# Kernel optimization log

Measured on AMD Instinct MI355X. Metric: run time of the kernel, lower is better.

## Reference

```python
import jax, jax.numpy as jnp
import numpy as np
from math import exp

C1 = 0.01 ** 2
C2 = 0.03 ** 2
WINDOW_SIZE = 11
SIGMA = 1.5

def make_window(window_size, channel, sigma=SIGMA):
    g = np.array([exp(-(x - window_size // 2) ** 2 / float(2 * sigma ** 2))
                  for x in range(window_size)], dtype=np.float32)
    g = g / g.sum()
    w2d = np.outer(g, g).astype(np.float32)  # [ws, ws]
    # depthwise kernel, OIHW with I=1 per group: [C, 1, ws, ws]
    return jnp.asarray(np.broadcast_to(w2d, (channel, 1, window_size, window_size)).copy())

def depthwise_conv(x, window, pad):
    C = x.shape[1]
    return jax.lax.conv_general_dilated(
        x, window, window_strides=(1, 1),
        padding=[(pad, pad), (pad, pad)],
        feature_group_count=C,
        dimension_numbers=('NCHW', 'OIHW', 'NCHW'))

def setup_inputs() -> dict:
    key = jax.random.key(0)
    k1, k2 = jax.random.split(key)
    B, C, H, W = 16, 3, 512, 512
    img1 = jax.random.uniform(k1, (B, C, H, W), dtype=jnp.float32)
    img2 = jax.random.uniform(k2, (B, C, H, W), dtype=jnp.float32)
    window = make_window(WINDOW_SIZE, C)
    return {"img1": img1, "img2": img2, "window": window}

def reference(img1, img2, window):
    pad = WINDOW_SIZE // 2
    mu1 = depthwise_conv(img1, window, pad)
    mu2 = depthwise_conv(img2, window, pad)
    mu1_sq = mu1 * mu1
    mu2_sq = mu2 * mu2
    mu1_mu2 = mu1 * mu2
    sigma1_sq = depthwise_conv(img1 * img1, window, pad) - mu1_sq
    sigma2_sq = depthwise_conv(img2 * img2, window, pad) - mu2_sq
    sigma12 = depthwise_conv(img1 * img2, window, pad) - mu1_mu2
    ssim_cs = (2 * sigma12 + C2) / (sigma1_sq + sigma2_sq + C2)
    ssim_l = (2 * mu1_mu2 + C1) / (mu1_sq + mu2_sq + C1)
    ssim_map = ssim_l * ssim_cs
    return jnp.mean(ssim_map)
```

## Files before the change

### kernel.cpp

```cpp
#include <hip/hip_runtime.h>


#define IMG_H 512
#define IMG_W 512
#define N_IMG 48
#define WS 11
#define PAD 5
#define CHUNK 16
#define NCHUNK (IMG_H / CHUNK)
#define NBLK (N_IMG * NCHUNK)
#define RING 12
#define OFF 6
#define VSW 524

__global__ __launch_bounds__(256, 4) void ssim_partial_kernel(
    const float* __restrict__ img1,
    const float* __restrict__ img2,
    const float* __restrict__ window,
    float* __restrict__ partial)
{
    __shared__ float vs[2][5][VSW];
    __shared__ float wred[4];

    const int tid = threadIdx.x;
    const int bc  = blockIdx.x;
    const int r0  = blockIdx.y * CHUNK;
    const int col = tid * 2;

    float g[WS];
    {
        const float g5  = sqrtf(window[5 * WS + 5]);
        const float inv = 1.0f / g5;
#pragma unroll
        for (int j = 0; j < WS; ++j) g[j] = window[5 * WS + j] * inv;
    }
    const float C1v = 0.01f * 0.01f;
    const float C2v = 0.03f * 0.03f;

    const float* __restrict__ p1 = img1 + (size_t)bc * (IMG_H * IMG_W);
    const float* __restrict__ p2 = img2 + (size_t)bc * (IMG_H * IMG_W);

    {
        float* vflat = &vs[0][0][0];
        for (int i = tid; i < 2 * 5 * VSW; i += 256) vflat[i] = 0.0f;
    }
    __syncthreads();

    float rx1a[RING], rx1b[RING], rx2a[RING], rx2b[RING];
#pragma unroll
    for (int i = 0; i < RING; ++i) { rx1a[i]=0.f; rx1b[i]=0.f; rx2a[i]=0.f; rx2b[i]=0.f; }

#pragma unroll
    for (int i = 0; i < 10; ++i) {
        const int rr = r0 - PAD + i;
        float a0=0.f, a1=0.f, b0=0.f, b1=0.f;
        if (rr >= 0 && rr < IMG_H) {
            const float2 u1 = *(const float2*)(p1 + rr * IMG_W + col);
            const float2 u2 = *(const float2*)(p2 + rr * IMG_W + col);
            a0 = u1.x; a1 = u1.y; b0 = u2.x; b1 = u2.y;
        }
        rx1a[2+i] = a0; rx1b[2+i] = a1; rx2a[2+i] = b0; rx2b[2+i] = b1;
    }

    float acc = 0.0f;

    for (int step = 0; step < CHUNK / 2; ++step) {
        const int R = r0 + step * 2;

#pragma unroll
        for (int i = 0; i < RING - 2; ++i) {
            rx1a[i] = rx1a[i+2]; rx1b[i] = rx1b[i+2];
            rx2a[i] = rx2a[i+2]; rx2b[i] = rx2b[i+2];
        }
#pragma unroll
        for (int j = 0; j < 2; ++j) {
            const int rr = R + PAD + j;
            float a0=0.f, a1=0.f, b0=0.f, b1=0.f;
            if (rr < IMG_H) {
                const float2 u1 = *(const float2*)(p1 + rr * IMG_W + col);
                const float2 u2 = *(const float2*)(p2 + rr * IMG_W + col);
                a0 = u1.x; a1 = u1.y; b0 = u2.x; b1 = u2.y;
            }
            rx1a[10+j] = a0; rx1b[10+j] = a1; rx2a[10+j] = b0; rx2b[10+j] = b1;
        }

#pragma unroll
        for (int j = 0; j < 2; ++j) {
            float v1a=0.f, v2a=0.f, v11a=0.f, v22a=0.f, v12a=0.f;
            float v1b=0.f, v2b=0.f, v11b=0.f, v22b=0.f, v12b=0.f;
#pragma unroll
            for (int i = 0; i < WS; ++i) {
                const float w  = g[i];
                const float x1 = rx1a[i+j], x2 = rx2a[i+j];
                const float t1 = w * x1,    t2 = w * x2;
                v1a += t1; v2a += t2;
                v11a = fmaf(t1, x1, v11a);
                v22a = fmaf(t2, x2, v22a);
                v12a = fmaf(t1, x2, v12a);
                const float y1 = rx1b[i+j], y2 = rx2b[i+j];
                const float s1 = w * y1,    s2 = w * y2;
                v1b += s1; v2b += s2;
                v11b = fmaf(s1, y1, v11b);
                v22b = fmaf(s2, y2, v22b);
                v12b = fmaf(s1, y2, v12b);
            }
            *(float2*)&vs[j][0][OFF + col] = make_float2(v1a,  v1b);
            *(float2*)&vs[j][1][OFF + col] = make_float2(v2a,  v2b);
            *(float2*)&vs[j][2][OFF + col] = make_float2(v11a, v11b);
            *(float2*)&vs[j][3][OFF + col] = make_float2(v22a, v22b);
            *(float2*)&vs[j][4][OFF + col] = make_float2(v12a, v12b);
        }
        __syncthreads();

#pragma unroll
        for (int j = 0; j < 2; ++j) {
            float hv[2][5];
#pragma unroll
            for (int p = 0; p < 5; ++p) {
                const float2* q = (const float2*)&vs[j][p][col];
                const float2 f0=q[0], f1=q[1], f2=q[2], f3=q[3],
                             f4=q[4], f5=q[5], f6=q[6];
                const float b[14] = {f0.x,f0.y,f1.x,f1.y,f2.x,f2.y,f3.x,f3.y,
                                     f4.x,f4.y,f5.x,f5.y,f6.x,f6.y};
                float s0 = 0.f, s1 = 0.f;
#pragma unroll
                for (int i = 0; i < WS; ++i) {
                    s0 = fmaf(g[i], b[i+1], s0);
                    s1 = fmaf(g[i], b[i+2], s1);
                }
                hv[0][p] = s0; hv[1][p] = s1;
            }
#pragma unroll
            for (int k = 0; k < 2; ++k) {
                const float mu1 = hv[k][0], mu2 = hv[k][1];
                const float mu1s = mu1 * mu1;
                const float mu2s = mu2 * mu2;
                const float mu12 = mu1 * mu2;
                const float sg1  = hv[k][2] - mu1s;
                const float sg2  = hv[k][3] - mu2s;
                const float sg12 = hv[k][4] - mu12;
                const float num  = (2.f * mu12 + C1v) * (2.f * sg12 + C2v);
                const float den  = (mu1s + mu2s + C1v) * (sg1 + sg2 + C2v);
                acc += num / den;
            }
        }
        __syncthreads();
    }

#pragma unroll
    for (int off = 32; off > 0; off >>= 1)
        acc += __shfl_down(acc, off);
    if ((tid & 63) == 0) wred[tid >> 6] = acc;
    __syncthreads();
    if (tid == 0) {
        const float s = wred[0] + wred[1] + wred[2] + wred[3];
        partial[blockIdx.y * N_IMG + blockIdx.x] = s;
    }
}

__global__ __launch_bounds__(256) void ssim_reduce_kernel(
    const float* __restrict__ partial, float* __restrict__ out)
{
    __shared__ double wred[4];
    const int tid = threadIdx.x;
    double s = 0.0;
    for (int i = tid; i < NBLK; i += 256) s += (double)partial[i];
#pragma unroll
    for (int off = 32; off > 0; off >>= 1)
        s += __shfl_down(s, off);
    if ((tid & 63) == 0) wred[tid >> 6] = s;
    __syncthreads();
    if (tid == 0) {
        const double total = wred[0] + wred[1] + wred[2] + wred[3];
        out[0] = (float)(total / (double)((size_t)N_IMG * IMG_H * IMG_W));
    }
}

extern "C" void kernel_launch(void* const* d_in, const int* in_sizes, int n_in,
                              void* d_out, int out_size, void* d_ws, size_t ws_size,
                              hipStream_t stream) {
    const float* img1   = (const float*)d_in[0];
    const float* img2   = (const float*)d_in[1];
    const float* window = (const float*)d_in[2];
    float* out     = (float*)d_out;
    float* partial = (float*)d_ws;

    dim3 grid(N_IMG, NCHUNK);
    ssim_partial_kernel<<<grid, 256, 0, stream>>>(img1, img2, window, partial);
    ssim_reduce_kernel<<<1, 256, 0, stream>>>(partial, out);
}
```

Measured before the change: 163.9 us.

## Merge sigma1/sigma2 planes, double-buffer LDS, and use fast reciprocal

Result: slower. 236.6 us (+44.3%).

```diff
diff --git a/kernel.cpp b/kernel.cpp
--- a/kernel.cpp
+++ b/kernel.cpp
@@ -13,13 +13,13 @@
 #define OFF 6
 #define VSW 524
 
-__global__ __launch_bounds__(256, 4) void ssim_partial_kernel(
+__global__ __launch_bounds__(256, 3) void ssim_partial_kernel(
     const float* __restrict__ img1,
     const float* __restrict__ img2,
     const float* __restrict__ window,
     float* __restrict__ partial)
 {
-    __shared__ float vs[2][5][VSW];
+    __shared__ float vs[2][2][4][VSW];
     __shared__ float wred[4];
 
     const int tid = threadIdx.x;
@@ -40,84 +40,94 @@
     const float* __restrict__ p1 = img1 + (size_t)bc * (IMG_H * IMG_W);
     const float* __restrict__ p2 = img2 + (size_t)bc * (IMG_H * IMG_W);
 
-    {
-        float* vflat = &vs[0][0][0];
-        for (int i = tid; i < 2 * 5 * VSW; i += 256) vflat[i] = 0.0f;
+    for (int i = tid; i < 2 * 2 * 4 * 12; i += 256) {
+        const int pr = i / 12, h = i % 12;
+        const int e  = (h < OFF) ? h : (512 + h);
+        (&vs[0][0][0][0])[pr * VSW + e] = 0.0f;
     }
     __syncthreads();
 
-    float rx1a[RING], rx1b[RING], rx2a[RING], rx2b[RING];
-#pragma unroll
-    for (int i = 0; i < RING; ++i) { rx1a[i]=0.f; rx1b[i]=0.f; rx2a[i]=0.f; rx2b[i]=0.f; }
+    float r1a[RING], r1b[RING], r2a[RING], r2b[RING];
+    float rsa[RING], rsb[RING], rpa[RING], rpb[RING];
+#pragma unroll
+    for (int i = 0; i < RING; ++i) {
+        r1a[i]=0.f; r1b[i]=0.f; r2a[i]=0.f; r2b[i]=0.f;
+        rsa[i]=0.f; rsb[i]=0.f; rpa[i]=0.f; rpb[i]=0.f;
+    }
 
 #pragma unroll
     for (int i = 0; i < 10; ++i) {
         const int rr = r0 - PAD + i;
-        float a0=0.f, a1=0.f, b0=0.f, b1=0.f;
+        float a1=0.f, b1=0.f, a2=0.f, b2=0.f;
         if (rr >= 0 && rr < IMG_H) {
             const float2 u1 = *(const float2*)(p1 + rr * IMG_W + col);
             const float2 u2 = *(const float2*)(p2 + rr * IMG_W + col);
-            a0 = u1.x; a1 = u1.y; b0 = u2.x; b1 = u2.y;
-        }
-        rx1a[2+i] = a0; rx1b[2+i] = a1; rx2a[2+i] = b0; rx2b[2+i] = b1;
+            a1 = u1.x; b1 = u1.y; a2 = u2.x; b2 = u2.y;
+        }
+        r1a[2+i] = a1; r1b[2+i] = b1; r2a[2+i] = a2; r2b[2+i] = b2;
+        rsa[2+i] = fmaf(a1, a1, a2 * a2);
+        rsb[2+i] = fmaf(b1, b1, b2 * b2);
+        rpa[2+i] = a1 * a2;
+        rpb[2+i] = b1 * b2;
     }
 
     float acc = 0.0f;
 
+#pragma unroll
     for (int step = 0; step < CHUNK / 2; ++step) {
-        const int R = r0 + step * 2;
+        const int R   = r0 + step * 2;
+        const int buf = step & 1;
 
 #pragma unroll
         for (int i = 0; i < RING - 2; ++i) {
-            rx1a[i] = rx1a[i+2]; rx1b[i] = rx1b[i+2];
-            rx2a[i] = rx2a[i+2]; rx2b[i] = rx2b[i+2];
+            r1a[i]=r1a[i+2]; r1b[i]=r1b[i+2]; r2a[i]=r2a[i+2]; r2b[i]=r2b[i+2];
+            rsa[i]=rsa[i+2]; rsb[i]=rsb[i+2]; rpa[i]=rpa[i+2]; rpb[i]=rpb[i+2];
         }
 #pragma unroll
         for (int j = 0; j < 2; ++j) {
             const int rr = R + PAD + j;
-            float a0=0.f, a1=0.f, b0=0.f, b1=0.f;
+            float a1=0.f, b1=0.f, a2=0.f, b2=0.f;
             if (rr < IMG_H) {
                 const float2 u1 = *(const float2*)(p1 + rr * IMG_W + col);
                 const float2 u2 = *(const float2*)(p2 + rr * IMG_W + col);
-                a0 = u1.x; a1 = u1.y; b0 = u2.x; b1 = u2.y;
-            }
-            rx1a[10+j] = a0; rx1b[10+j] = a1; rx2a[10+j] = b0; rx2b[10+j] = b1;
+                a1 = u1.x; b1 = u1.y; a2 = u2.x; b2 = u2.y;
+            }
+            r1a[10+j] = a1; r1b[10+j] = b1; r2a[10+j] = a2; r2b[10+j] = b2;
+            rsa[10+j] = fmaf(a1, a1, a2 * a2);
+            rsb[10+j] = fmaf(b1, b1, b2 * b2);
+            rpa[10+j] = a1 * a2;
+            rpb[10+j] = b1 * b2;
         }
 
 #pragma unroll
         for (int j = 0; j < 2; ++j) {
-            float v1a=0.f, v2a=0.f, v11a=0.f, v22a=0.f, v12a=0.f;
-            float v1b=0.f, v2b=0.f, v11b=0.f, v22b=0.f, v12b=0.f;
+            float v1a=0.f, v2a=0.f, vsa_=0.f, vpa_=0.f;
+            float v1b=0.f, v2b=0.f, vsb_=0.f, vpb_=0.f;
 #pragma unroll
             for (int i = 0; i < WS; ++i) {
-                const float w  = g[i];
-                const float x1 = rx1a[i+j], x2 = rx2a[i+j];
-                const float t1 = w * x1,    t2 = w * x2;
-                v1a += t1; v2a += t2;
-                v11a = fmaf(t1, x1, v11a);
-                v22a = fmaf(t2, x2, v22a);
-                v12a = fmaf(t1, x2, v12a);
-                const float y1 = rx1b[i+j], y2 = rx2b[i+j];
-                const float s1 = w * y1,    s2 = w * y2;
-                v1b += s1; v2b += s2;
-                v11b = fmaf(s1, y1, v11b);
-                v22b = fmaf(s2, y2, v22b);
-                v12b = fmaf(s1, y2, v12b);
-            }
-            *(float2*)&vs[j][0][OFF + col] = make_float2(v1a,  v1b);
-            *(float2*)&vs[j][1][OFF + col] = make_float2(v2a,  v2b);
-            *(float2*)&vs[j][2][OFF + col] = make_float2(v11a, v11b);
-            *(float2*)&vs[j][3][OFF + col] = make_float2(v22a, v22b);
-            *(float2*)&vs[j][4][OFF + col] = make_float2(v12a, v12b);
+                const float w = g[i];
+                v1a = fmaf(w, r1a[i+j], v1a);
+                v2a = fmaf(w, r2a[i+j], v2a);
+                vsa_ = fmaf(w, rsa[i+j], vsa_);
+                vpa_ = fmaf(w, rpa[i+j], vpa_);
+                v1b = fmaf(w, r1b[i+j], v1b);
+                v2b = fmaf(w, r2b[i+j], v2b);
+                vsb_ = fmaf(w, rsb[i+j], vsb_);
+                vpb_ = fmaf(w, rpb[i+j], vpb_);
+            }
+            *(float2*)&vs[buf][j][0][OFF + col] = make_float2(v1a,  v1b);
+            *(float2*)&vs[buf][j][1][OFF + col] = make_float2(v2a,  v2b);
+            *(float2*)&vs[buf][j][2][OFF + col] = make_float2(vsa_, vsb_);
+            *(float2*)&vs[buf][j][3][OFF + col] = make_float2(vpa_, vpb_);
         }
         __syncthreads();
 
 #pragma unroll
         for (int j = 0; j < 2; ++j) {
-            float hv[2][5];
-#pragma unroll
-            for (int p = 0; p < 5; ++p) {
-                const float2* q = (const float2*)&vs[j][p][col];
+            float hv[2][4];
+#pragma unroll
+            for (int p = 0; p < 4; ++p) {
+                const float2* q = (const float2*)&vs[buf][j][p][col];
                 const float2 f0=q[0], f1=q[1], f2=q[2], f3=q[3],
                              f4=q[4], f5=q[5], f6=q[6];
                 const float b[14] = {f0.x,f0.y,f1.x,f1.y,f2.x,f2.y,f3.x,f3.y,
@@ -133,18 +143,19 @@
 #pragma unroll
             for (int k = 0; k < 2; ++k) {
                 const float mu1 = hv[k][0], mu2 = hv[k][1];
+                const float hs  = hv[k][2], hp  = hv[k][3];
                 const float mu1s = mu1 * mu1;
                 const float mu2s = mu2 * mu2;
                 const float mu12 = mu1 * mu2;
-                const float sg1  = hv[k][2] - mu1s;
-                const float sg2  = hv[k][3] - mu2s;
-                const float sg12 = hv[k][4] - mu12;
+                const float sgs  = hs - mu1s - mu2s;
+                const float sg12 = hp - mu12;
                 const float num  = (2.f * mu12 + C1v) * (2.f * sg12 + C2v);
-                const float den  = (mu1s + mu2s + C1v) * (sg1 + sg2 + C2v);
-                acc += num / den;
-            }
-        }
-        __syncthreads();
+                const float den  = (mu1s + mu2s + C1v) * (sgs + C2v);
+                float r = __builtin_amdgcn_rcpf(den);
+                r = r * fmaf(-den, r, 2.0f);
+                acc = fmaf(num, r, acc);
+            }
+        }
     }
 
 #pragma unroll
```

## Merge variance terms, use fast reciprocal, fold final reduction into atomics

Applied to the files above, without the earlier changes.

New measurement: 155.8 us. -5.0%, faster.

```diff
diff --git a/kernel.cpp b/kernel.cpp
--- a/kernel.cpp
+++ b/kernel.cpp
@@ -8,18 +8,18 @@
 #define PAD 5
 #define CHUNK 16
 #define NCHUNK (IMG_H / CHUNK)
-#define NBLK (N_IMG * NCHUNK)
 #define RING 12
 #define OFF 6
 #define VSW 524
+#define INV_NPX (1.0f / (48.0f * 512.0f * 512.0f))
 
 __global__ __launch_bounds__(256, 4) void ssim_partial_kernel(
     const float* __restrict__ img1,
     const float* __restrict__ img2,
     const float* __restrict__ window,
-    float* __restrict__ partial)
+    float* __restrict__ out)
 {
-    __shared__ float vs[2][5][VSW];
+    __shared__ float vs[2][4][VSW];
     __shared__ float wred[4];
 
     const int tid = threadIdx.x;
@@ -42,7 +42,7 @@
 
     {
         float* vflat = &vs[0][0][0];
-        for (int i = tid; i < 2 * 5 * VSW; i += 256) vflat[i] = 0.0f;
+        for (int i = tid; i < 2 * 4 * VSW; i += 256) vflat[i] = 0.0f;
     }
     __syncthreads();
 
@@ -86,37 +86,34 @@
 
 #pragma unroll
         for (int j = 0; j < 2; ++j) {
-            float v1a=0.f, v2a=0.f, v11a=0.f, v22a=0.f, v12a=0.f;
-            float v1b=0.f, v2b=0.f, v11b=0.f, v22b=0.f, v12b=0.f;
+            float v1a=0.f, v2a=0.f, vsa=0.f, vpa=0.f;
+            float v1b=0.f, v2b=0.f, vsb=0.f, vpb=0.f;
 #pragma unroll
             for (int i = 0; i < WS; ++i) {
                 const float w  = g[i];
                 const float x1 = rx1a[i+j], x2 = rx2a[i+j];
                 const float t1 = w * x1,    t2 = w * x2;
                 v1a += t1; v2a += t2;
-                v11a = fmaf(t1, x1, v11a);
-                v22a = fmaf(t2, x2, v22a);
-                v12a = fmaf(t1, x2, v12a);
+                vsa = fmaf(t1, x1, fmaf(t2, x2, vsa));
+                vpa = fmaf(t1, x2, vpa);
                 const float y1 = rx1b[i+j], y2 = rx2b[i+j];
                 const float s1 = w * y1,    s2 = w * y2;
                 v1b += s1; v2b += s2;
-                v11b = fmaf(s1, y1, v11b);
-                v22b = fmaf(s2, y2, v22b);
-                v12b = fmaf(s1, y2, v12b);
+                vsb = fmaf(s1, y1, fmaf(s2, y2, vsb));
+                vpb = fmaf(s1, y2, vpb);
             }
-            *(float2*)&vs[j][0][OFF + col] = make_float2(v1a,  v1b);
-            *(float2*)&vs[j][1][OFF + col] = make_float2(v2a,  v2b);
-            *(float2*)&vs[j][2][OFF + col] = make_float2(v11a, v11b);
-            *(float2*)&vs[j][3][OFF + col] = make_float2(v22a, v22b);
-            *(float2*)&vs[j][4][OFF + col] = make_float2(v12a, v12b);
+            *(float2*)&vs[j][0][OFF + col] = make_float2(v1a, v1b);
+            *(float2*)&vs[j][1][OFF + col] = make_float2(v2a, v2b);
+            *(float2*)&vs[j][2][OFF + col] = make_float2(vsa, vsb);
+            *(float2*)&vs[j][3][OFF + col] = make_float2(vpa, vpb);
         }
         __syncthreads();
 
 #pragma unroll
         for (int j = 0; j < 2; ++j) {
-            float hv[2][5];
+            float hv[2][4];
 #pragma unroll
-            for (int p = 0; p < 5; ++p) {
+            for (int p = 0; p < 4; ++p) {
                 const float2* q = (const float2*)&vs[j][p][col];
                 const float2 f0=q[0], f1=q[1], f2=q[2], f3=q[3],
                              f4=q[4], f5=q[5], f6=q[6];
@@ -133,15 +130,17 @@
 #pragma unroll
             for (int k = 0; k < 2; ++k) {
                 const float mu1 = hv[k][0], mu2 = hv[k][1];
+                const float hs  = hv[k][2], hp  = hv[k][3];
                 const float mu1s = mu1 * mu1;
                 const float mu2s = mu2 * mu2;
                 const float mu12 = mu1 * mu2;
-                const float sg1  = hv[k][2] - mu1s;
-                const float sg2  = hv[k][3] - mu2s;
-                const float sg12 = hv[k][4] - mu12;
+                const float sgs  = hs - mu1s - mu2s;
+                const float sg12 = hp - mu12;
                 const float num  = (2.f * mu12 + C1v) * (2.f * sg12 + C2v);
-                const float den  = (mu1s + mu2s + C1v) * (sg1 + sg2 + C2v);
-                acc += num / den;
+                const float den  = (mu1s + mu2s + C1v) * (sgs + C2v);
+                float r = __builtin_amdgcn_rcpf(den);
+                r = r * fmaf(-den, r, 2.0f);
+                acc = fmaf(num, r, acc);
             }
         }
         __syncthreads();
@@ -153,26 +152,8 @@
     if ((tid & 63) == 0) wred[tid >> 6] = acc;
     __syncthreads();
     if (tid == 0) {
-        const float s = wred[0] + wred[1] + wred[2] + wred[3];
-        partial[blockIdx.y * N_IMG + blockIdx.x] = s;
-    }
-}
-
-__global__ __launch_bounds__(256) void ssim_reduce_kernel(
-    const float* __restrict__ partial, float* __restrict__ out)
-{
-    __shared__ double wred[4];
-    const int tid = threadIdx.x;
-    double s = 0.0;
-    for (int i = tid; i < NBLK; i += 256) s += (double)partial[i];
-#pragma unroll
-    for (int off = 32; off > 0; off >>= 1)
-        s += __shfl_down(s, off);
-    if ((tid & 63) == 0) wred[tid >> 6] = s;
-    __syncthreads();
-    if (tid == 0) {
-        const double total = wred[0] + wred[1] + wred[2] + wred[3];
-        out[0] = (float)(total / (double)((size_t)N_IMG * IMG_H * IMG_W));
+        const float s = (wred[0] + wred[1]) + (wred[2] + wred[3]);
+        atomicAdd(out, s * INV_NPX);
     }
 }
 
@@ -182,10 +163,9 @@
     const float* img1   = (const float*)d_in[0];
     const float* img2   = (const float*)d_in[1];
     const float* window = (const float*)d_in[2];
-    float* out     = (float*)d_out;
-    float* partial = (float*)d_ws;
+    float* out = (float*)d_out;
 
+    hipMemsetAsync(out, 0, sizeof(float), stream);
     dim3 grid(N_IMG, NCHUNK);
-    ssim_partial_kernel<<<grid, 256, 0, stream>>>(img1, img2, window, partial);
-    ssim_reduce_kernel<<<1, 256, 0, stream>>>(partial, out);
+    ssim_partial_kernel<<<grid, 256, 0, stream>>>(img1, img2, window, out);
 }
```
